# Optimization experiments

Measured on AMD Instinct MI355X. Metric: run time of the kernel, lower is better.

Reference implementation:

```python
import jax, jax.numpy as jnp
import numpy as np

N_HEAD = 16

def setup_inputs() -> dict:
    key = jax.random.key(0)
    k1, k2, k3, k4, k5 = jax.random.split(key, 5)
    B, T, C = 2, 2048, 1024
    x = jax.random.normal(k1, (B, T, C), dtype=jnp.float32)
    s = 0.02
    W_attn = jax.random.normal(k2, (C, 3 * C), dtype=jnp.float32) * s
    b_attn = jnp.zeros((3 * C,), dtype=jnp.float32)
    W_proj = jax.random.normal(k3, (C, C), dtype=jnp.float32) * s
    b_proj = jnp.zeros((C,), dtype=jnp.float32)
    return {"x": x, "W_attn": W_attn, "b_attn": b_attn, "W_proj": W_proj, "b_proj": b_proj}

def reference(x, W_attn, b_attn, W_proj, b_proj):
    B, T, C = x.shape
    H = N_HEAD
    hd = C // H
    qkv = x @ W_attn + b_attn                      # (B,T,3C)
    q, k, v = jnp.split(qkv, 3, axis=-1)
    # (B,T,C) -> (B,H,T,hd)
    def to_heads(t):
        return t.reshape(B, T, H, hd).transpose(0, 2, 1, 3)
    q, k, v = to_heads(q), to_heads(k), to_heads(v)
    scale = 1.0 / jnp.sqrt(jnp.asarray(hd, dtype=x.dtype))
    att = jnp.einsum('bhqd,bhkd->bhqk', q, k) * scale  # (B,H,T,T)
    causal = jnp.tril(jnp.ones((T, T), dtype=bool))
    att = jnp.where(causal[None, None], att, -jnp.inf)
    att = jax.nn.softmax(att, axis=-1)
    y = jnp.einsum('bhqk,bhkd->bhqd', att, v)          # (B,H,T,hd)
    y = y.transpose(0, 2, 1, 3).reshape(B, T, C)
    return y @ W_proj + b_proj
```

## Files before the change

kernel.cpp:

```cpp
#include <hip/hip_runtime.h>

#define N_HEAD 16

typedef __attribute__((ext_vector_type(8))) __bf16 bf16x8;
typedef __attribute__((ext_vector_type(8))) short  s16x8;
typedef __attribute__((ext_vector_type(4))) short  s16x4;
typedef __attribute__((ext_vector_type(4))) float  f32x4;
typedef __attribute__((ext_vector_type(4))) unsigned u32x4;

#if __has_builtin(__builtin_amdgcn_exp2f)
#define EXP2(x) __builtin_amdgcn_exp2f(x)
#else
#define EXP2(x) exp2f(x)
#endif
#if __has_builtin(__builtin_amdgcn_rcpf)
#define RCP(x) __builtin_amdgcn_rcpf(x)
#else
#define RCP(x) (1.0f / (x))
#endif

static __device__ __forceinline__ short f2bf(float f) {
    unsigned u = __builtin_bit_cast(unsigned, f);
    unsigned r = (u + 0x7FFFu + ((u >> 16) & 1u)) >> 16;
    return (short)r;
}

static __device__ __forceinline__ unsigned cvt_pk_bf16(float lo, float hi) {
    unsigned d;
    asm("v_cvt_pk_bf16_f32 %0, %1, %2" : "=v"(d) : "v"(lo), "v"(hi));
    return d;
}

static __device__ __forceinline__ void gload_lds16(const void* g, void* l) {
    __builtin_amdgcn_global_load_lds(
        (const __attribute__((address_space(1))) void*)g,
        (__attribute__((address_space(3))) void*)l, 16, 0, 0);
}

#define BARX() do { asm volatile("" ::: "memory"); __builtin_amdgcn_s_barrier(); \
                    asm volatile("" ::: "memory"); } while (0)
#define VMCNT4() asm volatile("s_waitcnt vmcnt(4)" ::: "memory")
#define VMCNT0() asm volatile("s_waitcnt vmcnt(0)" ::: "memory")

__global__ __launch_bounds__(256) void prep(
    const float* __restrict__ X,  short* __restrict__ Xb,
    const float* __restrict__ Wa, short* __restrict__ Wat,
    const float* __restrict__ Wp, short* __restrict__ Wpt)
{
    __shared__ short Ts[64][72];
    const int bid = blockIdx.x, tid = threadIdx.x;
    if (bid < 2048) {
        size_t base = ((size_t)bid * 256 + tid) * 8;
        float4 f0 = *(const float4*)&X[base];
        float4 f1 = *(const float4*)&X[base + 4];
        s16x8 o;
        o[0] = f2bf(f0.x); o[1] = f2bf(f0.y); o[2] = f2bf(f0.z); o[3] = f2bf(f0.w);
        o[4] = f2bf(f1.x); o[5] = f2bf(f1.y); o[6] = f2bf(f1.z); o[7] = f2bf(f1.w);
        *(s16x8*)&Xb[base] = o;
        return;
    }
    const float* W; short* Wt; int N, n0, k0;
    if (bid < 2816) { int rr = bid - 2048; W = Wa; Wt = Wat; N = 3072; n0 = (rr % 48) * 64; k0 = (rr / 48) * 64; }
    else            { int rr = bid - 2816; W = Wp; Wt = Wpt; N = 1024; n0 = (rr % 16) * 64; k0 = (rr / 16) * 64; }
    const int r = tid >> 4, c4 = (tid & 15) * 4;
#pragma unroll
    for (int i = 0; i < 4; ++i) {
        int row = r + i * 16;
        float4 f = *(const float4*)&W[(size_t)(k0 + row) * N + n0 + c4];
        s16x4 s = { f2bf(f.x), f2bf(f.y), f2bf(f.z), f2bf(f.w) };
        *(s16x4*)&Ts[row][c4] = s;
    }
    __syncthreads();
#pragma unroll
    for (int i = 0; i < 4; ++i) {
        int row = r + i * 16;
        s16x4 s = { Ts[c4 + 0][row], Ts[c4 + 1][row], Ts[c4 + 2][row], Ts[c4 + 3][row] };
        *(s16x4*)&Wt[(size_t)(n0 + row) * 1024 + k0 + c4] = s;
    }
}

__global__ __launch_bounds__(256) void qkv_gemm(
    const short* __restrict__ Xb,
    const short* __restrict__ Wt,
    const float* __restrict__ bias,
    short* __restrict__ Qo, short* __restrict__ Ko, short* __restrict__ Vo)
{
    __shared__ short As[3 * 4096];
    __shared__ short Bs[3 * 4096];
    const int tid = threadIdx.x, wave = tid >> 6, lane = tid & 63;
    const int row0 = blockIdx.x * 128, col0 = blockIdx.y * 128;
    const int srow = wave * 16 + (lane >> 2);
    const int sc = (((lane & 3) ^ ((lane >> 3) & 3)) * 8);
    const short* aS = Xb + (size_t)(row0 + srow) * 1024 + sc;
    const short* bS = Wt + (size_t)(col0 + srow) * 1024 + sc;
    const int woff = wave * 512;
    const int wr = (wave >> 1) * 64, wc = (wave & 1) * 64;
    const int arow = lane & 15, g = lane >> 4;
    const int foff = (g ^ ((arow >> 1) & 3)) * 8;

    f32x4 acc[4][4] = {};

#define STAGE(T, BUF) do { const size_t _k = (size_t)(T) * 32; \
    gload_lds16(aS + _k,             As + (BUF) * 4096 + woff); \
    gload_lds16(aS + _k + 64 * 1024, As + (BUF) * 4096 + woff + 2048); \
    gload_lds16(bS + _k,             Bs + (BUF) * 4096 + woff); \
    gload_lds16(bS + _k + 64 * 1024, Bs + (BUF) * 4096 + woff + 2048); \
} while (0)

#define COMPUTE(BUF) do { \
    bf16x8 af[4], bfr[4]; \
    _Pragma("unroll") \
    for (int i = 0; i < 4; ++i) af[i]  = *(const bf16x8*)&As[(BUF) * 4096 + (wr + i * 16 + arow) * 32 + foff]; \
    _Pragma("unroll") \
    for (int j = 0; j < 4; ++j) bfr[j] = *(const bf16x8*)&Bs[(BUF) * 4096 + (wc + j * 16 + arow) * 32 + foff]; \
    _Pragma("unroll") \
    for (int i = 0; i < 4; ++i) \
        _Pragma("unroll") \
        for (int j = 0; j < 4; ++j) \
            acc[i][j] = __builtin_amdgcn_mfma_f32_16x16x32_bf16(af[i], bfr[j], acc[i][j], 0, 0, 0); \
} while (0)

    STAGE(0, 0); STAGE(1, 1);
    VMCNT4(); BARX();

    int cur = 0;
    for (int t = 0; t < 30; ++t) {
        int nbuf = cur + 2; if (nbuf >= 3) nbuf -= 3;
        STAGE(t + 2, nbuf);
        COMPUTE(cur);
        VMCNT4(); BARX();
        cur = (cur == 2) ? 0 : cur + 1;
    }
    COMPUTE(cur); VMCNT0(); BARX();
    cur = (cur == 2) ? 0 : cur + 1;
    COMPUTE(cur);
#undef STAGE
#undef COMPUTE

    const int which = col0 >> 10;
    const int bb = row0 >> 11;
    const int ccol = arow, crow = g * 4;
#pragma unroll
    for (int j = 0; j < 4; ++j) {
        int n = col0 + wc + j * 16 + ccol;
        float bv = bias[n];
        int nc = n & 1023, head = nc >> 6, hd = nc & 63;
        if (which == 0) {
#pragma unroll
            for (int i = 0; i < 4; ++i) {
                int t0 = (row0 & 2047) + wr + i * 16 + crow;
#pragma unroll
                for (int r = 0; r < 4; ++r)
                    Qo[((size_t)(bb * N_HEAD + head) * 2048 + t0 + r) * 64 + hd] =
                        f2bf((acc[i][j][r] + bv) * 0.18033688f);
            }
        } else if (which == 1) {
#pragma unroll
            for (int i = 0; i < 4; ++i) {
                int t0 = (row0 & 2047) + wr + i * 16 + crow;
#pragma unroll
                for (int r = 0; r < 4; ++r)
                    Ko[((size_t)(bb * N_HEAD + head) * 2048 + t0 + r) * 64 + hd] =
                        f2bf(acc[i][j][r] + bv);
            }
        } else {
#pragma unroll
            for (int i = 0; i < 4; ++i) {
                int t0 = (row0 & 2047) + wr + i * 16 + crow;
                s16x4 ov = { f2bf(acc[i][j][0] + bv), f2bf(acc[i][j][1] + bv),
                             f2bf(acc[i][j][2] + bv), f2bf(acc[i][j][3] + bv) };
                *(s16x4*)&Vo[((size_t)(bb * N_HEAD + head) * 64 + hd) * 2048 + t0] = ov;
            }
        }
    }
}

__global__ __launch_bounds__(256) void attn_kernel(
    const short* __restrict__ Q, const short* __restrict__ K,
    const short* __restrict__ Vt, short* __restrict__ Y)
{
    __shared__ short Ks[2][64 * 64];
    __shared__ short Vs[2][64 * 64];
    const int bh = blockIdx.x;
    const int by = blockIdx.y, ba = by >> 3, bq = by & 7;
    const int qt = (ba == 0) ? bq : (ba == 1) ? (31 - bq) : (ba == 2) ? (8 + bq) : (23 - bq);
    const int q0 = qt * 64;
    const int b = bh >> 4, h = bh & 15;
    const short* Qh = Q  + (size_t)bh * 2048 * 64;
    const short* Kh = K  + (size_t)bh * 2048 * 64;
    const short* Vh = Vt + (size_t)bh * 64 * 2048;
    const int tid = threadIdx.x, wave = tid >> 6, lane = tid & 63;
    const int qrow0 = q0 + wave * 16;
    const int arow = lane & 15, g = lane >> 4;

    const int rho = wave * 16 + (lane >> 3);
    const int kappa = ((rho >> 5) << 5) | (((rho >> 2) & 3) << 3)
                    | (((rho >> 4) & 1) << 2) | (rho & 3);
    const int xchunk = 8 * ((lane & 7) ^ (rho & 7));
    const short* kSrc = Kh + (size_t)kappa * 64 + xchunk;
    const short* vSrc = Vh + (size_t)rho * 2048 + xchunk;

    bf16x8 qfr[2];
#pragma unroll
    for (int c = 0; c < 2; ++c)
        qfr[c] = *(const bf16x8*)&Qh[(size_t)(qrow0 + arow) * 64 + c * 32 + (g * 8)];

    f32x4 o[4] = {};
    float lsum = 0.f;

    const int nt = qt + 1;

    gload_lds16(kSrc,            Ks[0] + wave * 1024);
    gload_lds16(kSrc + 1024,     Ks[0] + wave * 1024 + 512);
    gload_lds16(vSrc,            Vs[0] + wave * 1024);
    gload_lds16(vSrc + 8 * 2048, Vs[0] + wave * 1024 + 512);
    __syncthreads();

    int cur = 0;
    for (int t = 0; t < nt; ++t) {
        const int kt = t << 6;
        if (t + 1 < nt) {
            const int kn = kt + 64;
            short* kD = Ks[cur ^ 1] + wave * 1024;
            short* vD = Vs[cur ^ 1] + wave * 1024;
            gload_lds16(kSrc + (size_t)kn * 64,        kD);
            gload_lds16(kSrc + (size_t)kn * 64 + 1024, kD + 512);
            gload_lds16(vSrc + kn,                     vD);
            gload_lds16(vSrc + kn + 8 * 2048,          vD + 512);
        }
        if (kt <= qrow0 + 15) {
            const short* Kc = Ks[cur];
            const short* Vc = Vs[cur];
            const bool need_mask = (kt + 64) > qrow0;
            f32x4 s[4] = {};
#pragma unroll
            for (int kc = 0; kc < 4; ++kc) {
                int krow = kc * 16 + arow;
                int xr = krow & 7;
#pragma unroll
                for (int c = 0; c < 2; ++c) {
                    bf16x8 kf = *(const bf16x8*)&Kc[krow * 64 + (((c * 4 + g) ^ xr) * 8)];
                    s[kc] = __builtin_amdgcn_mfma_f32_16x16x32_bf16(kf, qfr[c], s[kc], 0, 0, 0);
                }
            }
            if (need_mask) {
                int q = qrow0 + arow;
#pragma unroll
                for (int kc = 0; kc < 4; ++kc) {
                    int keyb = kt + ((kc >> 1) << 5) + (g << 3) + ((kc & 1) << 2);
#pragma unroll
                    for (int r = 0; r < 4; ++r)
                        if (keyb + r > q) s[kc][r] = -3.0e38f;
                }
            }
            unsigned pa[8];
#pragma unroll
            for (int kc = 0; kc < 4; ++kc) {
                float p0 = EXP2(s[kc][0]);
                float p1 = EXP2(s[kc][1]);
                float p2 = EXP2(s[kc][2]);
                float p3 = EXP2(s[kc][3]);
                lsum += (p0 + p1) + (p2 + p3);
                pa[kc * 2 + 0] = cvt_pk_bf16(p0, p1);
                pa[kc * 2 + 1] = cvt_pk_bf16(p2, p3);
            }
#pragma unroll
            for (int c = 0; c < 2; ++c) {
                bf16x8 pb = __builtin_bit_cast(bf16x8,
                    (u32x4){ pa[4 * c], pa[4 * c + 1], pa[4 * c + 2], pa[4 * c + 3] });
#pragma unroll
                for (int j = 0; j < 4; ++j) {
                    int d = j * 16 + arow;
                    bf16x8 vf = *(const bf16x8*)&Vc[d * 64 + (((c * 4 + g) ^ (d & 7)) * 8)];
                    o[j] = __builtin_amdgcn_mfma_f32_16x16x32_bf16(vf, pb, o[j], 0, 0, 0);
                }
            }
        }
        __syncthreads();
        cur ^= 1;
    }

    {
        float l = lsum;
        l += __shfl_xor(l, 16);
        l += __shfl_xor(l, 32);
        float li = RCP(l);
        int t = qrow0 + arow;
#pragma unroll
        for (int j = 0; j < 4; ++j) {
            s16x4 ov = { f2bf(o[j][0] * li), f2bf(o[j][1] * li),
                         f2bf(o[j][2] * li), f2bf(o[j][3] * li) };
            *(s16x4*)&Y[((size_t)(b * 2048 + t)) * 1024 + h * 64 + j * 16 + 4 * g] = ov;
        }
    }
}

__global__ __launch_bounds__(256) void proj_gemm(
    const short* __restrict__ Yb,
    const short* __restrict__ Wpt,
    const float* __restrict__ bias,
    float* __restrict__ Out)
{
    __shared__ short As[2][4096];
    __shared__ short Bs[2][4096];
    const int tid = threadIdx.x, wave = tid >> 6, lane = tid & 63;
    const int row0 = blockIdx.x * 128, col0 = blockIdx.y * 128;
    const int srow = wave * 16 + (lane >> 2);
    const int sc = (((lane & 3) ^ ((lane >> 3) & 3)) * 8);
    const short* aS = Yb  + (size_t)(row0 + srow) * 1024 + sc;
    const short* bS = Wpt + (size_t)(col0 + srow) * 1024 + sc;
    const int woff = wave * 512;
    const int wr = (wave >> 1) * 64, wc = (wave & 1) * 64;
    const int arow = lane & 15, g = lane >> 4;
    const int foff = (g ^ ((arow >> 1) & 3)) * 8;

    f32x4 acc[4][4] = {};

    gload_lds16(aS,             As[0] + woff);
    gload_lds16(aS + 64 * 1024, As[0] + woff + 2048);
    gload_lds16(bS,             Bs[0] + woff);
    gload_lds16(bS + 64 * 1024, Bs[0] + woff + 2048);
    __syncthreads();

    int cur = 0;
    for (int k0 = 0; k0 < 1024; k0 += 32) {
        if (k0 + 32 < 1024) {
            gload_lds16(aS + k0 + 32,             As[cur ^ 1] + woff);
            gload_lds16(aS + k0 + 32 + 64 * 1024, As[cur ^ 1] + woff + 2048);
            gload_lds16(bS + k0 + 32,             Bs[cur ^ 1] + woff);
            gload_lds16(bS + k0 + 32 + 64 * 1024, Bs[cur ^ 1] + woff + 2048);
        }
        bf16x8 af[4], bfr[4];
#pragma unroll
        for (int i = 0; i < 4; ++i) af[i]  = *(const bf16x8*)&As[cur][(wr + i * 16 + arow) * 32 + foff];
#pragma unroll
        for (int j = 0; j < 4; ++j) bfr[j] = *(const bf16x8*)&Bs[cur][(wc + j * 16 + arow) * 32 + foff];
#pragma unroll
        for (int i = 0; i < 4; ++i)
#pragma unroll
            for (int j = 0; j < 4; ++j)
                acc[i][j] = __builtin_amdgcn_mfma_f32_16x16x32_bf16(af[i], bfr[j], acc[i][j], 0, 0, 0);
        __syncthreads();
        cur ^= 1;
    }

    const int ccol = arow, crow = g * 4;
#pragma unroll
    for (int i = 0; i < 4; ++i)
#pragma unroll
        for (int j = 0; j < 4; ++j)
#pragma unroll
            for (int r = 0; r < 4; ++r) {
                int m = row0 + wr + i * 16 + crow + r;
                int n = col0 + wc + j * 16 + ccol;
                Out[(size_t)m * 1024 + n] = acc[i][j][r] + bias[n];
            }
}

extern "C" void kernel_launch(void* const* d_in, const int* in_sizes, int n_in,
                              void* d_out, int out_size, void* d_ws, size_t ws_size,
                              hipStream_t stream) {
    const float* x      = (const float*)d_in[0];
    const float* W_attn = (const float*)d_in[1];
    const float* b_attn = (const float*)d_in[2];
    const float* W_proj = (const float*)d_in[3];
    const float* b_proj = (const float*)d_in[4];
    float* out = (float*)d_out;

    short* Xb  = (short*)d_ws;
    short* Wat = Xb + 4194304;
    short* Wpt = Wat + 3145728;
    short* qb  = Wpt + 1048576;
    short* kb  = qb + 4194304;
    short* vb  = kb + 4194304;
    short* yb  = Xb;

    prep<<<3072, 256, 0, stream>>>(x, Xb, W_attn, Wat, W_proj, Wpt);
    qkv_gemm<<<dim3(32, 24), 256, 0, stream>>>(Xb, Wat, b_attn, qb, kb, vb);
    attn_kernel<<<dim3(32, 32), 256, 0, stream>>>(qb, kb, vb, yb);
    proj_gemm<<<dim3(32, 8), 256, 0, stream>>>(yb, Wpt, b_proj, out);
}
```

Measured before the change: 104.3 us.

## Use two waves per attention block with 32 query rows each and MFMA priority

The attention kernel now runs 128 threads (2 waves) per 64-query block, and each wave handles two 16-row query fragments, so every K/V fragment read from LDS feeds two MFMAs. Each thread stages twice as much K/V data per tile to keep the tile size unchanged. s_setprio is raised around the MFMA sections to favour matrix issue. The change cuts LDS traffic per FLOP, but it doubles accumulator registers per wave and halves the waves available to hide latency per block.

```diff
diff --git a/kernel.cpp b/kernel.cpp
--- a/kernel.cpp
+++ b/kernel.cpp
@@ -175,12 +175,12 @@
     }
 }
 
-__global__ __launch_bounds__(256) void attn_kernel(
+__global__ __launch_bounds__(128) void attn_kernel(
     const short* __restrict__ Q, const short* __restrict__ K,
     const short* __restrict__ Vt, short* __restrict__ Y)
 {
-    __shared__ short Ks[2][64 * 64];
-    __shared__ short Vs[2][64 * 64];
+    __shared__ short Ks[2][4096];
+    __shared__ short Vs[2][4096];
     const int bh = blockIdx.x;
     const int by = blockIdx.y, ba = by >> 3, bq = by & 7;
     const int qt = (ba == 0) ? bq : (ba == 1) ? (31 - bq) : (ba == 2) ? (8 + bq) : (23 - bq);
@@ -190,49 +190,52 @@
     const short* Kh = K  + (size_t)bh * 2048 * 64;
     const short* Vh = Vt + (size_t)bh * 64 * 2048;
     const int tid = threadIdx.x, wave = tid >> 6, lane = tid & 63;
-    const int qrow0 = q0 + wave * 16;
+    const int qrow0 = q0 + wave * 32;
     const int arow = lane & 15, g = lane >> 4;
 
-    const int rho = wave * 16 + (lane >> 3);
+    const int rho = wave * 32 + (lane >> 3);
     const int kappa = ((rho >> 5) << 5) | (((rho >> 2) & 3) << 3)
                     | (((rho >> 4) & 1) << 2) | (rho & 3);
     const int xchunk = 8 * ((lane & 7) ^ (rho & 7));
     const short* kSrc = Kh + (size_t)kappa * 64 + xchunk;
     const short* vSrc = Vh + (size_t)rho * 2048 + xchunk;
 
-    bf16x8 qfr[2];
-#pragma unroll
-    for (int c = 0; c < 2; ++c)
-        qfr[c] = *(const bf16x8*)&Qh[(size_t)(qrow0 + arow) * 64 + c * 32 + (g * 8)];
-
-    f32x4 o[4] = {};
-    float lsum = 0.f;
+#define STAGE_KV(BUF, KT) do { \
+    short* kD = Ks[BUF] + wave * 2048; \
+    short* vD = Vs[BUF] + wave * 2048; \
+    const short* kS = kSrc + (size_t)(KT) * 64; \
+    const short* vS = vSrc + (KT); \
+    gload_lds16(kS,        kD);        gload_lds16(kS + 1024, kD + 512); \
+    gload_lds16(kS + 256,  kD + 1024); gload_lds16(kS + 1280, kD + 1536); \
+    gload_lds16(vS,             vD);        gload_lds16(vS + 8  * 2048, vD + 512); \
+    gload_lds16(vS + 16 * 2048, vD + 1024); gload_lds16(vS + 24 * 2048, vD + 1536); \
+} while (0)
+
+    bf16x8 qfr[2][2];
+#pragma unroll
+    for (int qf = 0; qf < 2; ++qf)
+#pragma unroll
+        for (int c = 0; c < 2; ++c)
+            qfr[qf][c] = *(const bf16x8*)&Qh[(size_t)(qrow0 + qf * 16 + arow) * 64 + c * 32 + (g * 8)];
+
+    f32x4 o[2][4] = {};
+    float lsum[2] = {};
 
     const int nt = qt + 1;
 
-    gload_lds16(kSrc,            Ks[0] + wave * 1024);
-    gload_lds16(kSrc + 1024,     Ks[0] + wave * 1024 + 512);
-    gload_lds16(vSrc,            Vs[0] + wave * 1024);
-    gload_lds16(vSrc + 8 * 2048, Vs[0] + wave * 1024 + 512);
+    STAGE_KV(0, 0);
     __syncthreads();
 
     int cur = 0;
     for (int t = 0; t < nt; ++t) {
         const int kt = t << 6;
-        if (t + 1 < nt) {
-            const int kn = kt + 64;
-            short* kD = Ks[cur ^ 1] + wave * 1024;
-            short* vD = Vs[cur ^ 1] + wave * 1024;
-            gload_lds16(kSrc + (size_t)kn * 64,        kD);
-            gload_lds16(kSrc + (size_t)kn * 64 + 1024, kD + 512);
-            gload_lds16(vSrc + kn,                     vD);
-            gload_lds16(vSrc + kn + 8 * 2048,          vD + 512);
-        }
-        if (kt <= qrow0 + 15) {
+        if (t + 1 < nt) STAGE_KV(cur ^ 1, kt + 64);
+        if (kt <= qrow0 + 31) {
             const short* Kc = Ks[cur];
             const short* Vc = Vs[cur];
             const bool need_mask = (kt + 64) > qrow0;
-            f32x4 s[4] = {};
+            f32x4 s[2][4] = {};
+            __builtin_amdgcn_s_setprio(1);
 #pragma unroll
             for (int kc = 0; kc < 4; ++kc) {
                 int krow = kc * 16 + arow;
@@ -240,56 +243,72 @@
 #pragma unroll
                 for (int c = 0; c < 2; ++c) {
                     bf16x8 kf = *(const bf16x8*)&Kc[krow * 64 + (((c * 4 + g) ^ xr) * 8)];
-                    s[kc] = __builtin_amdgcn_mfma_f32_16x16x32_bf16(kf, qfr[c], s[kc], 0, 0, 0);
+#pragma unroll
+                    for (int qf = 0; qf < 2; ++qf)
+                        s[qf][kc] = __builtin_amdgcn_mfma_f32_16x16x32_bf16(kf, qfr[qf][c], s[qf][kc], 0, 0, 0);
                 }
             }
+            __builtin_amdgcn_s_setprio(0);
             if (need_mask) {
-                int q = qrow0 + arow;
+#pragma unroll
+                for (int qf = 0; qf < 2; ++qf) {
+                    int q = qrow0 + qf * 16 + arow;
+#pragma unroll
+                    for (int kc = 0; kc < 4; ++kc) {
+                        int keyb = kt + ((kc >> 1) << 5) + (g << 3) + ((kc & 1) << 2);
+#pragma unroll
+                        for (int r = 0; r < 4; ++r)
+                            if (keyb + r > q) s[qf][kc][r] = -3.0e38f;
+                    }
+                }
+            }
+            unsigned pa[2][8];
+#pragma unroll
+            for (int qf = 0; qf < 2; ++qf) {
 #pragma unroll
                 for (int kc = 0; kc < 4; ++kc) {
-                    int keyb = kt + ((kc >> 1) << 5) + (g << 3) + ((kc & 1) << 2);
-#pragma unroll
-                    for (int r = 0; r < 4; ++r)
-                        if (keyb + r > q) s[kc][r] = -3.0e38f;
+                    float p0 = EXP2(s[qf][kc][0]);
+                    float p1 = EXP2(s[qf][kc][1]);
+                    float p2 = EXP2(s[qf][kc][2]);
+                    float p3 = EXP2(s[qf][kc][3]);
+                    lsum[qf] += (p0 + p1) + (p2 + p3);
+                    pa[qf][kc * 2 + 0] = cvt_pk_bf16(p0, p1);
+                    pa[qf][kc * 2 + 1] = cvt_pk_bf16(p2, p3);
                 }
             }
-            unsigned pa[8];
-#pragma unroll
-            for (int kc = 0; kc < 4; ++kc) {
-                float p0 = EXP2(s[kc][0]);
-                float p1 = EXP2(s[kc][1]);
-                float p2 = EXP2(s[kc][2]);
-                float p3 = EXP2(s[kc][3]);
-                lsum += (p0 + p1) + (p2 + p3);
-                pa[kc * 2 + 0] = cvt_pk_bf16(p0, p1);
-                pa[kc * 2 + 1] = cvt_pk_bf16(p2, p3);
-            }
+            __builtin_amdgcn_s_setprio(1);
 #pragma unroll
             for (int c = 0; c < 2; ++c) {
-                bf16x8 pb = __builtin_bit_cast(bf16x8,
-                    (u32x4){ pa[4 * c], pa[4 * c + 1], pa[4 * c + 2], pa[4 * c + 3] });
+                bf16x8 pb0 = __builtin_bit_cast(bf16x8,
+                    (u32x4){ pa[0][4 * c], pa[0][4 * c + 1], pa[0][4 * c + 2], pa[0][4 * c + 3] });
+                bf16x8 pb1 = __builtin_bit_cast(bf16x8,
+                    (u32x4){ pa[1][4 * c], pa[1][4 * c + 1], pa[1][4 * c + 2], pa[1][4 * c + 3] });
 #pragma unroll
                 for (int j = 0; j < 4; ++j) {
                     int d = j * 16 + arow;
                     bf16x8 vf = *(const bf16x8*)&Vc[d * 64 + (((c * 4 + g) ^ (d & 7)) * 8)];
-                    o[j] = __builtin_amdgcn_mfma_f32_16x16x32_bf16(vf, pb, o[j], 0, 0, 0);
+                    o[0][j] = __builtin_amdgcn_mfma_f32_16x16x32_bf16(vf, pb0, o[0][j], 0, 0, 0);
+                    o[1][j] = __builtin_amdgcn_mfma_f32_16x16x32_bf16(vf, pb1, o[1][j], 0, 0, 0);
                 }
             }
+            __builtin_amdgcn_s_setprio(0);
         }
         __syncthreads();
         cur ^= 1;
     }
-
-    {
-        float l = lsum;
+#undef STAGE_KV
+
+#pragma unroll
+    for (int qf = 0; qf < 2; ++qf) {
+        float l = lsum[qf];
         l += __shfl_xor(l, 16);
         l += __shfl_xor(l, 32);
         float li = RCP(l);
-        int t = qrow0 + arow;
+        int t = qrow0 + qf * 16 + arow;
 #pragma unroll
         for (int j = 0; j < 4; ++j) {
-            s16x4 ov = { f2bf(o[j][0] * li), f2bf(o[j][1] * li),
-                         f2bf(o[j][2] * li), f2bf(o[j][3] * li) };
+            s16x4 ov = { f2bf(o[qf][j][0] * li), f2bf(o[qf][j][1] * li),
+                         f2bf(o[qf][j][2] * li), f2bf(o[qf][j][3] * li) };
             *(s16x4*)&Y[((size_t)(b * 2048 + t)) * 1024 + h * 64 + j * 16 + 4 * g] = ov;
         }
     }
@@ -377,6 +396,6 @@
 
     prep<<<3072, 256, 0, stream>>>(x, Xb, W_attn, Wat, W_proj, Wpt);
     qkv_gemm<<<dim3(32, 24), 256, 0, stream>>>(Xb, Wat, b_attn, qb, kb, vb);
-    attn_kernel<<<dim3(32, 32), 256, 0, stream>>>(qb, kb, vb, yb);
+    attn_kernel<<<dim3(32, 32), 128, 0, stream>>>(qb, kb, vb, yb);
     proj_gemm<<<dim3(32, 8), 256, 0, stream>>>(yb, Wpt, b_proj, out);
 }
```

Result: slower. 110.6 us (+6.1%).

## Prefetch K/V tiles two iterations ahead with explicit vmcnt waits

Applied to the files above, without the earlier changes.

The attention loop now stages the first two K/V tiles before the loop. Inside the loop, after a barrier, it issues the load for tile t+2 into the buffer that was just consumed. An explicit vmcnt wait (4 outstanding, or 0 on the tail) plus barrier replaces the plain __syncthreads, so the next tile's global-to-LDS copy has a whole iteration to complete. This adds a second barrier per iteration and relies on the vmcnt macros and the exact count of outstanding loads being correct.

```diff
diff --git a/kernel.cpp b/kernel.cpp
--- a/kernel.cpp
+++ b/kernel.cpp
@@ -200,6 +200,15 @@
     const short* kSrc = Kh + (size_t)kappa * 64 + xchunk;
     const short* vSrc = Vh + (size_t)rho * 2048 + xchunk;
 
+#define STAGE_KV(BUF, KT) do { \
+    short* kD = Ks[BUF] + wave * 1024; \
+    short* vD = Vs[BUF] + wave * 1024; \
+    gload_lds16(kSrc + (size_t)(KT) * 64,        kD); \
+    gload_lds16(kSrc + (size_t)(KT) * 64 + 1024, kD + 512); \
+    gload_lds16(vSrc + (KT),                     vD); \
+    gload_lds16(vSrc + (KT) + 8 * 2048,          vD + 512); \
+} while (0)
+
     bf16x8 qfr[2];
 #pragma unroll
     for (int c = 0; c < 2; ++c)
@@ -210,24 +219,13 @@
 
     const int nt = qt + 1;
 
-    gload_lds16(kSrc,            Ks[0] + wave * 1024);
-    gload_lds16(kSrc + 1024,     Ks[0] + wave * 1024 + 512);
-    gload_lds16(vSrc,            Vs[0] + wave * 1024);
-    gload_lds16(vSrc + 8 * 2048, Vs[0] + wave * 1024 + 512);
-    __syncthreads();
-
-    int cur = 0;
+    STAGE_KV(0, 0);
+    STAGE_KV(1, 64);
+    VMCNT4(); BARX();
+
     for (int t = 0; t < nt; ++t) {
         const int kt = t << 6;
-        if (t + 1 < nt) {
-            const int kn = kt + 64;
-            short* kD = Ks[cur ^ 1] + wave * 1024;
-            short* vD = Vs[cur ^ 1] + wave * 1024;
-            gload_lds16(kSrc + (size_t)kn * 64,        kD);
-            gload_lds16(kSrc + (size_t)kn * 64 + 1024, kD + 512);
-            gload_lds16(vSrc + kn,                     vD);
-            gload_lds16(vSrc + kn + 8 * 2048,          vD + 512);
-        }
+        const int cur = t & 1;
         if (kt <= qrow0 + 15) {
             const short* Kc = Ks[cur];
             const short* Vc = Vs[cur];
@@ -276,9 +274,16 @@
                 }
             }
         }
-        __syncthreads();
-        cur ^= 1;
-    }
+        BARX();
+        if (t + 2 < nt) {
+            STAGE_KV(cur, kt + 128);
+            VMCNT4();
+        } else {
+            VMCNT0();
+        }
+        BARX();
+    }
+#undef STAGE_KV
 
     {
         float l = lsum;
```

Result: no change. 103.3 us (median of 3 runs) (-1.0%).
